# Optimization experiments

Hardware: AMD Instinct MI355X
Metric: run time of the kernel (lower is better)

The kernel has to match this reference:

```python
import jax, jax.numpy as jnp
import numpy as np

# aero table grids (degrees)
A_LO, A_HI = -20.0, 90.0
B_LO, B_HI = -30.0, 30.0
E_LO, E_HI = -25.0, 25.0


def _idx(x, lo, hi, n):
    t = jnp.clip((x - lo) / (hi - lo) * (n - 1), 0.0, float(n - 1))
    i0 = jnp.clip(t.astype(jnp.int32), 0, n - 2)
    return i0, t - i0


def _interp1(tab, x, lo, hi):
    i0, f = _idx(x, lo, hi, tab.shape[-1])
    return tab[..., i0] * (1.0 - f) + tab[..., i0 + 1] * f


def _interp2(tab, a, b):
    ia, fa = _idx(a, A_LO, A_HI, tab.shape[-2])
    ib, fb = _idx(b, B_LO, B_HI, tab.shape[-1])
    return (tab[:, ia, ib] * (1 - fa) * (1 - fb)
            + tab[:, ia + 1, ib] * fa * (1 - fb)
            + tab[:, ia, ib + 1] * (1 - fa) * fb
            + tab[:, ia + 1, ib + 1] * fa * fb)


def _interp3(tab, a, b, e):
    ia, fa = _idx(a, A_LO, A_HI, tab.shape[-3])
    ib, fb = _idx(b, B_LO, B_HI, tab.shape[-2])
    ie, fe = _idx(e, E_LO, E_HI, tab.shape[-1])
    out = 0.0
    for di, wa in ((0, 1 - fa), (1, fa)):
        for dj, wb in ((0, 1 - fb), (1, fb)):
            for dk, we in ((0, 1 - fe), (1, fe)):
                out = out + tab[:, ia + di, ib + dj, ie + dk] * (wa * wb * we)
    return out


def _nlplant(xu, tab3, tab2, tab1, tab_eta):
    g, m, Bspan, S, cbar = 32.17, 636.94, 30.0, 300.0, 11.32
    xcgr, xcg, Heng = 0.35, 0.25, 0.0
    Jy, Jxz, Jz, Jx = 55814.0, 982.0, 63100.0, 9496.0
    r2d = 180.0 / np.pi

    alt = xu[:, 2]
    phi, theta, psi = xu[:, 3], xu[:, 4], xu[:, 5]
    vt = jnp.maximum(xu[:, 6], 0.01)          # if vt < 0.01: vt = 0.01
    alpha, beta = xu[:, 7], xu[:, 8]
    a_deg, b_deg = alpha * r2d, beta * r2d
    P, Q, R = xu[:, 9], xu[:, 10], xu[:, 11]
    T, el, ail, rud, lef = xu[:, 12], xu[:, 13], xu[:, 14], xu[:, 15], xu[:, 16]
    dail, drud, dlef = ail / 21.5, rud / 30.0, 1.0 - lef / 25.0

    # --- Atmos ---
    tfac = 1.0 - 7.03e-06 * alt
    temp = jnp.where(alt >= 35000.0, 390.0, 519.0 * tfac)
    rho = 0.002377 * jnp.power(tfac, 4.14)
    qbar = 0.5 * rho * vt * vt
    ps = 1715.0 * rho * temp
    ps = jnp.where(ps == 0.0, 1715.0, ps)

    sa, ca = jnp.sin(alpha), jnp.cos(alpha)
    sb, cb = jnp.sin(beta), jnp.cos(beta)
    st, ct, tt = jnp.sin(theta), jnp.cos(theta), jnp.tan(theta)
    sphi, cphi = jnp.sin(phi), jnp.cos(phi)
    spsi, cpsi = jnp.sin(psi), jnp.cos(psi)

    U, V, W = vt * ca * cb, vt * sb, vt * sa * cb

    xd0 = U * (ct * cpsi) + V * (sphi * cpsi * st - cphi * spsi) + W * (cphi * st * cpsi + sphi * spsi)
    xd1 = U * (ct * spsi) + V * (sphi * spsi * st + cphi * cpsi) + W * (cphi * st * spsi - sphi * cpsi)
    xd2 = U * st - V * (sphi * ct) - W * (cphi * ct)
    xd3 = P + tt * (Q * sphi + R * cphi)
    xd4 = Q * cphi - R * sphi
    xd5 = (Q * sphi + R * cphi) / ct

    # --- aero table lookups ---
    v3 = _interp3(tab3, a_deg, b_deg, el)                    # [5,B]: Cx,Cz,Cm,Cn,Cl at el
    v30 = _interp3(tab3, a_deg, b_deg, jnp.zeros_like(el))   # [5,B]: at el=0
    v2 = _interp2(tab2, a_deg, b_deg)                        # [16,B]
    v1 = _interp1(tab1, a_deg, A_LO, A_HI)                   # [21,B]
    eta_el = _interp1(tab_eta, el, E_LO, E_HI)               # [B]

    Cx, Cz, Cm, Cn, Cl = v3[0], v3[1], v3[2], v3[3], v3[4]
    Cy = v2[0]
    (Cxq, Cyr, Cyp, Czq, Clr, Clp, Cmq, Cnr, Cnp,
     dCxq_lef, dCyr_lef, dCyp_lef, dCzq_lef, dClr_lef, dClp_lef,
     dCmq_lef, dCnr_lef, dCnp_lef, dCnbeta, dClbeta, dCm) = [v1[i] for i in range(21)]

    d_Cx_lef = v2[1] - v30[0]
    d_Cz_lef = v2[2] - v30[1]
    d_Cm_lef = v2[3] - v30[2]
    d_Cy_lef = v2[4] - v2[0]
    d_Cn_lef = v2[5] - v30[3]
    d_Cl_lef = v2[6] - v30[4]
    d_Cy_r30 = v2[7] - v2[0]
    d_Cn_r30 = v2[8] - v30[3]
    d_Cl_r30 = v2[9] - v30[4]
    d_Cy_a20 = v2[10] - v2[0]
    d_Cy_a20_lef = v2[11] - v2[4]
    d_Cn_a20 = v2[12] - v30[3]
    d_Cn_a20_lef = v2[13] - v2[5]
    d_Cl_a20 = v2[14] - v30[4]
    d_Cl_a20_lef = v2[15] - v2[6]
    d_Cm_ds = 0.0

    # --- total coefficients ---
    c2v = 1.0 / (2.0 * vt)
    dXdQ = cbar * c2v * (Cxq + dCxq_lef * dlef)
    Cx_tot = Cx + d_Cx_lef * dlef + dXdQ * Q
    dZdQ = cbar * c2v * (Czq + dCzq_lef * dlef)
    Cz_tot = Cz + d_Cz_lef * dlef + dZdQ * Q
    dMdQ = cbar * c2v * (Cmq + dCmq_lef * dlef)
    Cm_tot = Cm * eta_el + Cz_tot * (xcgr - xcg) + d_Cm_lef * dlef + dMdQ * Q + dCm + d_Cm_ds
    dYdail = d_Cy_a20 + d_Cy_a20_lef * dlef
    dYdR = Bspan * c2v * (Cyr + dCyr_lef * dlef)
    dYdP = Bspan * c2v * (Cyp + dCyp_lef * dlef)
    Cy_tot = Cy + d_Cy_lef * dlef + dYdail * dail + d_Cy_r30 * drud + dYdR * R + dYdP * P
    dNdail = d_Cn_a20 + d_Cn_a20_lef * dlef
    dNdR = Bspan * c2v * (Cnr + dCnr_lef * dlef)
    dNdP = Bspan * c2v * (Cnp + dCnp_lef * dlef)
    Cn_tot = (Cn + d_Cn_lef * dlef - Cy_tot * (xcgr - xcg) * (cbar / Bspan)
              + dNdail * dail + d_Cn_r30 * drud + dNdR * R + dNdP * P + dCnbeta * b_deg)
    dLdail = d_Cl_a20 + d_Cl_a20_lef * dlef
    dLdR = Bspan * c2v * (Clr + dClr_lef * dlef)
    dLdP = Bspan * c2v * (Clp + dClp_lef * dlef)
    Cl_tot = (Cl + d_Cl_lef * dlef + dLdail * dail + d_Cl_r30 * drud
              + dLdR * R + dLdP * P + dClbeta * b_deg)

    # --- body-axis accelerations ---
    qS_m = qbar * S / m
    Udot = R * V - Q * W - g * st + qS_m * Cx_tot + T / m
    Vdot = P * W - R * U + g * ct * sphi + qS_m * Cy_tot
    Wdot = Q * U - P * V + g * ct * cphi + qS_m * Cz_tot
    vt_dot = (U * Udot + V * Vdot + W * Wdot) / vt
    alpha_dot = (U * Wdot - W * Udot) / (U * U + W * W)
    beta_dot = (Vdot * vt - V * vt_dot) / (vt * vt * cb)

    # --- moments ---
    L_tot = Cl_tot * qbar * S * Bspan
    M_tot = Cm_tot * qbar * S * cbar
    N_tot = Cn_tot * qbar * S * Bspan
    denom = Jx * Jz - Jxz * Jxz
    P_dot = (Jz * L_tot + Jxz * N_tot - (Jz * (Jz - Jy) + Jxz * Jxz) * Q * R
             + Jxz * (Jx - Jy + Jz) * P * Q + Jxz * Q * Heng) / denom
    Q_dot = (M_tot + (Jz - Jx) * P * R - Jxz * (P * P - R * R) - R * Heng) / Jy
    R_dot = (Jx * N_tot + Jxz * L_tot + (Jx * (Jx - Jy) + Jxz * Jxz) * P * Q
             - Jxz * (Jx - Jy + Jz) * Q * R + Jx * Q * Heng) / denom

    xdot12 = jnp.stack([xd0, xd1, xd2, xd3, xd4, xd5,
                        vt_dot, alpha_dot, beta_dot, P_dot, Q_dot, R_dot], axis=1)
    return jnp.concatenate([xdot12, jnp.zeros((xu.shape[0], 5), xu.dtype)], axis=1)


def setup_inputs() -> dict:
    key = jax.random.key(0)
    k0, k1, k2, k3, k4 = jax.random.split(key, 5)
    Bn = 1 << 20
    u = jax.random.uniform(k0, (Bn, 17), dtype=jnp.float32)
    lo = jnp.array([0., 0., 0., -1., -1., -3., 300., -0.30, -0.5, -2., -2., -2.,
                    1000., -25., -21.5, -30., 0.], dtype=jnp.float32)
    hi = jnp.array([1000., 1000., 40000., 1., 1., 3., 900., 0.75, 0.5, 2., 2., 2.,
                    19000., 25., 21.5, 30., 25.], dtype=jnp.float32)
    xu = lo + u * (hi - lo)
    tab3 = 0.1 * jax.random.normal(k1, (5, 20, 19, 5), dtype=jnp.float32)
    tab2 = 0.05 * jax.random.normal(k2, (16, 20, 19), dtype=jnp.float32)
    tab1 = 0.1 * jax.random.normal(k3, (21, 20), dtype=jnp.float32)
    tab_eta = 1.0 + 0.05 * jax.random.normal(k4, (5,), dtype=jnp.float32)
    return {"xu": xu, "tab3": tab3, "tab2": tab2, "tab1": tab1, "tab_eta": tab_eta}


def reference(xu, tab3, tab2, tab1, tab_eta):
    return _nlplant(xu, tab3, tab2, tab1, tab_eta)
```

## Files before the change

### kernel.cpp

```cpp
#include <hip/hip_runtime.h>

#define BLOCK 1024
#define ROWS_PER_BLOCK 1024

__device__ __forceinline__ void idx_of(float x, float lo, float inv_range_times_nm1,
                                       int n, int& i0, float& f) {
    float t = (x - lo) * inv_range_times_nm1;
    t = fminf(fmaxf(t, 0.0f), (float)(n - 1));
    int i = (int)t;
    if (i > n - 2) i = n - 2;
    i0 = i;
    f = t - (float)i;
}

__global__ __launch_bounds__(BLOCK, 1)
void nlplant_kernel(const float* __restrict__ xu,
                    const float* __restrict__ tab3,
                    const float* __restrict__ tab2,
                    const float* __restrict__ tab1,
                    const float* __restrict__ tab_eta,
                    float* __restrict__ out, int nrows)
{
    __shared__ __align__(16) float s_t3a[1900 * 4];
    __shared__ __align__(16) float s_t3b[1900];
    __shared__ __align__(16) float s_tab2[380 * 20];
    __shared__ __align__(16) float s_tab1[428];
    __shared__ __align__(16) float s_io[512 * 17];

    const int tid = threadIdx.x;

#pragma unroll
    for (int c = 0; c < 5; ++c) {
        for (int idx = tid; idx < 1900; idx += BLOCK) {
            const float v = tab3[c * 1900 + idx];
            if (c < 4) s_t3a[(idx << 2) + c] = v;
            else       s_t3b[idx] = v;
        }
    }
    if (tid < 380) {
#pragma unroll
        for (int ch = 0; ch < 16; ++ch)
            s_tab2[tid * 20 + ch] = tab2[ch * 380 + tid];
    }
    if (tid < 420) {
        const int ch = tid / 20;
        const int ia = tid - ch * 20;
        s_tab1[ia * 21 + ch] = tab1[tid];
    }
    if (tid < 5) s_tab1[420 + tid] = tab_eta[tid];

    const int base = blockIdx.x * ROWS_PER_BLOCK;
    int remA = nrows - base;           if (remA < 0) remA = 0;
    const int rowsA = remA < 512 ? remA : 512;
    int remB = nrows - base - 512;     if (remB < 0) remB = 0;
    const int rowsB = remB < 512 ? remB : 512;

    if (rowsA == 512) {
        const float4* src = reinterpret_cast<const float4*>(xu + (size_t)base * 17);
        float4* dst = reinterpret_cast<float4*>(s_io);
        for (int k = tid; k < 2176; k += BLOCK) dst[k] = src[k];
    } else {
        for (int k = tid; k < rowsA * 17; k += BLOCK) s_io[k] = xu[(size_t)base * 17 + k];
    }
    __syncthreads();

    const int half = tid >> 9;
    const int l = tid & 511;
    const bool active = (half == 0) ? (l < rowsA) : (l < rowsB);

    float x[17];
#pragma unroll
    for (int j = 0; j < 17; ++j) x[j] = 1.0f;

    if (half == 0 && l < rowsA) {
#pragma unroll
        for (int j = 2; j < 17; ++j) x[j] = s_io[l * 17 + j];
    }
    __syncthreads();

    if (rowsB == 512) {
        const float4* src = reinterpret_cast<const float4*>(xu + (size_t)(base + 512) * 17);
        float4* dst = reinterpret_cast<float4*>(s_io);
        for (int k = tid; k < 2176; k += BLOCK) dst[k] = src[k];
    } else {
        for (int k = tid; k < rowsB * 17; k += BLOCK) s_io[k] = xu[(size_t)(base + 512) * 17 + k];
    }
    __syncthreads();
    if (half == 1 && l < rowsB) {
#pragma unroll
        for (int j = 2; j < 17; ++j) x[j] = s_io[l * 17 + j];
    }

    const float g = 32.17f, m_ = 636.94f, Bs = 30.0f, S = 300.0f, cbar = 11.32f;
    const float xcgr = 0.35f, xcg = 0.25f;
    const float Jy = 55814.0f, Jxz = 982.0f, Jz = 63100.0f, Jx = 9496.0f;
    const float r2d = 57.29577951308232f;

    const float alt = x[2], phi = x[3], theta = x[4], psi = x[5];
    const float vt = fmaxf(x[6], 0.01f);
    const float alpha = x[7], beta = x[8];
    const float a_deg = alpha * r2d, b_deg = beta * r2d;
    const float P = x[9], Q = x[10], R = x[11];
    const float T = x[12], el = x[13], ail = x[14], rud = x[15], lef = x[16];

    const float dail = ail * (1.0f / 21.5f);
    const float drud = rud * (1.0f / 30.0f);
    const float dlef = 1.0f - lef * (1.0f / 25.0f);

    const float tfac = 1.0f - 7.03e-6f * alt;
    const float rho = 0.002377f * __expf(4.14f * __logf(tfac));
    const float qbar = 0.5f * rho * vt * vt;

    float sa, ca, sb, cb, st, ct, sphi, cphi, spsi, cpsi;
    __sincosf(alpha, &sa, &ca);
    __sincosf(beta, &sb, &cb);
    __sincosf(theta, &st, &ct);
    __sincosf(phi, &sphi, &cphi);
    __sincosf(psi, &spsi, &cpsi);
    const float tt = st / ct;

    int ia, ib, ie; float fa, fb, fe;
    idx_of(a_deg, -20.0f, 19.0f / 110.0f, 20, ia, fa);
    idx_of(b_deg, -30.0f, 18.0f / 60.0f, 19, ib, fb);
    idx_of(el,    -25.0f,  4.0f / 50.0f,  5, ie, fe);

    const float wa[2] = {1.0f - fa, fa};
    const float wb[2] = {1.0f - fb, fb};
    const float we[2] = {1.0f - fe, fe};

    float v3c[5]  = {0, 0, 0, 0, 0};
    float v30c[5] = {0, 0, 0, 0, 0};
#pragma unroll
    for (int di = 0; di < 2; ++di) {
#pragma unroll
        for (int dj = 0; dj < 2; ++dj) {
            const float wab = wa[di] * wb[dj];
            const int pb3 = ((ia + di) * 19 + (ib + dj)) * 5;
#pragma unroll
            for (int dk = 0; dk < 2; ++dk) {
                const int idx = pb3 + ie + dk;
                const float4 q = *reinterpret_cast<const float4*>(&s_t3a[idx << 2]);
                const float q4 = s_t3b[idx];
                const float w = wab * we[dk];
                v3c[0] += q.x * w; v3c[1] += q.y * w; v3c[2] += q.z * w;
                v3c[3] += q.w * w; v3c[4] += q4 * w;
            }
            const int zidx = pb3 + 2;
            const float4 q0 = *reinterpret_cast<const float4*>(&s_t3a[zidx << 2]);
            const float q04 = s_t3b[zidx];
            v30c[0] += q0.x * wab; v30c[1] += q0.y * wab; v30c[2] += q0.z * wab;
            v30c[3] += q0.w * wab; v30c[4] += q04 * wab;
        }
    }

    float v2c[16];
    {
        const float w00 = wa[0] * wb[0], w01 = wa[0] * wb[1];
        const float w10 = wa[1] * wb[0], w11 = wa[1] * wb[1];
        const float4* p00 = reinterpret_cast<const float4*>(&s_tab2[(ia * 19 + ib) * 20]);
        const float4* p01 = reinterpret_cast<const float4*>(&s_tab2[(ia * 19 + ib + 1) * 20]);
        const float4* p10 = reinterpret_cast<const float4*>(&s_tab2[((ia + 1) * 19 + ib) * 20]);
        const float4* p11 = reinterpret_cast<const float4*>(&s_tab2[((ia + 1) * 19 + ib + 1) * 20]);
#pragma unroll
        for (int q = 0; q < 4; ++q) {
            const float4 a = p00[q], b = p01[q], c = p10[q], d = p11[q];
            v2c[4 * q + 0] = a.x * w00 + b.x * w01 + c.x * w10 + d.x * w11;
            v2c[4 * q + 1] = a.y * w00 + b.y * w01 + c.y * w10 + d.y * w11;
            v2c[4 * q + 2] = a.z * w00 + b.z * w01 + c.z * w10 + d.z * w11;
            v2c[4 * q + 3] = a.w * w00 + b.w * w01 + c.w * w10 + d.w * w11;
        }
    }

    float v1c[21];
    {
        const float* r0 = &s_tab1[ia * 21];
        const float* r1 = &s_tab1[(ia + 1) * 21];
#pragma unroll
        for (int c = 0; c < 21; ++c) v1c[c] = r0[c] * wa[0] + r1[c] * wa[1];
    }
    const float eta_el = s_tab1[420 + ie] * we[0] + s_tab1[421 + ie] * we[1];

    const float Cx = v3c[0], Cz = v3c[1], Cm = v3c[2], Cn = v3c[3], Cl = v3c[4];
    const float Cy = v2c[0];
    const float Cxq = v1c[0], Cyr = v1c[1], Cyp = v1c[2], Czq = v1c[3], Clr = v1c[4];
    const float Clp = v1c[5], Cmq = v1c[6], Cnr = v1c[7], Cnp = v1c[8];
    const float dCxq_lef = v1c[9], dCyr_lef = v1c[10], dCyp_lef = v1c[11];
    const float dCzq_lef = v1c[12], dClr_lef = v1c[13], dClp_lef = v1c[14];
    const float dCmq_lef = v1c[15], dCnr_lef = v1c[16], dCnp_lef = v1c[17];
    const float dCnbeta = v1c[18], dClbeta = v1c[19], dCm = v1c[20];

    const float d_Cx_lef = v2c[1] - v30c[0];
    const float d_Cz_lef = v2c[2] - v30c[1];
    const float d_Cm_lef = v2c[3] - v30c[2];
    const float d_Cy_lef = v2c[4] - v2c[0];
    const float d_Cn_lef = v2c[5] - v30c[3];
    const float d_Cl_lef = v2c[6] - v30c[4];
    const float d_Cy_r30 = v2c[7] - v2c[0];
    const float d_Cn_r30 = v2c[8] - v30c[3];
    const float d_Cl_r30 = v2c[9] - v30c[4];
    const float d_Cy_a20 = v2c[10] - v2c[0];
    const float d_Cy_a20_lef = v2c[11] - v2c[4];
    const float d_Cn_a20 = v2c[12] - v30c[3];
    const float d_Cn_a20_lef = v2c[13] - v2c[5];
    const float d_Cl_a20 = v2c[14] - v30c[4];
    const float d_Cl_a20_lef = v2c[15] - v2c[6];

    const float U = vt * ca * cb, V = vt * sb, W = vt * sa * cb;
    const float o0 = U * (ct * cpsi) + V * (sphi * cpsi * st - cphi * spsi) + W * (cphi * st * cpsi + sphi * spsi);
    const float o1 = U * (ct * spsi) + V * (sphi * spsi * st + cphi * cpsi) + W * (cphi * st * spsi - sphi * cpsi);
    const float o2 = U * st - V * (sphi * ct) - W * (cphi * ct);
    const float o3 = P + tt * (Q * sphi + R * cphi);
    const float o4 = Q * cphi - R * sphi;
    const float o5 = (Q * sphi + R * cphi) / ct;

    const float c2v = 1.0f / (2.0f * vt);
    const float cq = cbar * c2v, bq = Bs * c2v;
    const float dXdQ = cq * (Cxq + dCxq_lef * dlef);
    const float Cx_tot = Cx + d_Cx_lef * dlef + dXdQ * Q;
    const float dZdQ = cq * (Czq + dCzq_lef * dlef);
    const float Cz_tot = Cz + d_Cz_lef * dlef + dZdQ * Q;
    const float dMdQ = cq * (Cmq + dCmq_lef * dlef);
    const float Cm_tot = Cm * eta_el + Cz_tot * (xcgr - xcg) + d_Cm_lef * dlef + dMdQ * Q + dCm;
    const float dYdail = d_Cy_a20 + d_Cy_a20_lef * dlef;
    const float dYdR = bq * (Cyr + dCyr_lef * dlef);
    const float dYdP = bq * (Cyp + dCyp_lef * dlef);
    const float Cy_tot = Cy + d_Cy_lef * dlef + dYdail * dail + d_Cy_r30 * drud + dYdR * R + dYdP * P;
    const float dNdail = d_Cn_a20 + d_Cn_a20_lef * dlef;
    const float dNdR = bq * (Cnr + dCnr_lef * dlef);
    const float dNdP = bq * (Cnp + dCnp_lef * dlef);
    const float Cn_tot = Cn + d_Cn_lef * dlef - Cy_tot * ((xcgr - xcg) * (cbar / Bs))
                       + dNdail * dail + d_Cn_r30 * drud + dNdR * R + dNdP * P + dCnbeta * b_deg;
    const float dLdail = d_Cl_a20 + d_Cl_a20_lef * dlef;
    const float dLdR = bq * (Clr + dClr_lef * dlef);
    const float dLdP = bq * (Clp + dClp_lef * dlef);
    const float Cl_tot = Cl + d_Cl_lef * dlef + dLdail * dail + d_Cl_r30 * drud
                       + dLdR * R + dLdP * P + dClbeta * b_deg;

    const float qS = qbar * S;
    const float qS_m = qS * (1.0f / m_);
    const float Udot = R * V - Q * W - g * st + qS_m * Cx_tot + T * (1.0f / m_);
    const float Vdot = P * W - R * U + g * ct * sphi + qS_m * Cy_tot;
    const float Wdot = Q * U - P * V + g * ct * cphi + qS_m * Cz_tot;
    const float o6 = (U * Udot + V * Vdot + W * Wdot) / vt;
    const float o7 = (U * Wdot - W * Udot) / (U * U + W * W);
    const float o8 = (Vdot * vt - V * o6) / (vt * vt * cb);

    const float L_tot = Cl_tot * qS * Bs;
    const float M_tot = Cm_tot * qS * cbar;
    const float N_tot = Cn_tot * qS * Bs;
    const float denom = Jx * Jz - Jxz * Jxz;
    const float inv_denom = 1.0f / denom;
    const float o9  = (Jz * L_tot + Jxz * N_tot - (Jz * (Jz - Jy) + Jxz * Jxz) * Q * R
                      + Jxz * (Jx - Jy + Jz) * P * Q) * inv_denom;
    const float o10 = (M_tot + (Jz - Jx) * P * R - Jxz * (P * P - R * R)) * (1.0f / Jy);
    const float o11 = (Jx * N_tot + Jxz * L_tot + (Jx * (Jx - Jy) + Jxz * Jxz) * P * Q
                      - Jxz * (Jx - Jy + Jz) * Q * R) * inv_denom;

    float o[17] = {o0, o1, o2, o3, o4, o5, o6, o7, o8, o9, o10, o11,
                   0.0f, 0.0f, 0.0f, 0.0f, 0.0f};

    __syncthreads();
    if (half == 0 && active) {
#pragma unroll
        for (int j = 0; j < 17; ++j) s_io[l * 17 + j] = o[j];
    }
    __syncthreads();
    if (rowsA == 512) {
        const float4* src = reinterpret_cast<const float4*>(s_io);
        float4* dst = reinterpret_cast<float4*>(out + (size_t)base * 17);
        for (int k = tid; k < 2176; k += BLOCK) dst[k] = src[k];
    } else {
        for (int k = tid; k < rowsA * 17; k += BLOCK) out[(size_t)base * 17 + k] = s_io[k];
    }
    __syncthreads();
    if (half == 1 && active) {
#pragma unroll
        for (int j = 0; j < 17; ++j) s_io[l * 17 + j] = o[j];
    }
    __syncthreads();
    if (rowsB == 512) {
        const float4* src = reinterpret_cast<const float4*>(s_io);
        float4* dst = reinterpret_cast<float4*>(out + (size_t)(base + 512) * 17);
        for (int k = tid; k < 2176; k += BLOCK) dst[k] = src[k];
    } else {
        for (int k = tid; k < rowsB * 17; k += BLOCK) out[(size_t)(base + 512) * 17 + k] = s_io[k];
    }
}

extern "C" void kernel_launch(void* const* d_in, const int* in_sizes, int n_in,
                              void* d_out, int out_size, void* d_ws, size_t ws_size,
                              hipStream_t stream) {
    const float* xu      = (const float*)d_in[0];
    const float* tab3    = (const float*)d_in[1];
    const float* tab2    = (const float*)d_in[2];
    const float* tab1    = (const float*)d_in[3];
    const float* tab_eta = (const float*)d_in[4];
    float* out = (float*)d_out;

    const int nrows = in_sizes[0] / 17;
    const int grid = (nrows + ROWS_PER_BLOCK - 1) / ROWS_PER_BLOCK;
    nlplant_kernel<<<grid, BLOCK, 0, stream>>>(xu, tab3, tab2, tab1, tab_eta, out, nrows);
}
```

Measured before the change: 64.14 us.

## Process two full 1024-row passes per block with direct strided output stores

Each block now handles 2048 rows in two passes where every thread computes one row, instead of 1024 rows staged as two 512-row halves. This amortizes the per-block table load into shared memory over more rows and doubles the staging buffer. Output is now written directly from registers with strided scalar stores, dropping the shared-memory staging and the coalesced float4 store. Divisions are replaced by hardware reciprocal approximations and tab1 is padded to stride 28 for float4 reads. The strided global stores risk poor coalescing, the larger shared footprint may cut occupancy, and the reciprocals slightly change numerics.

```diff
diff --git a/kernel.cpp b/kernel.cpp
--- a/kernel.cpp
+++ b/kernel.cpp
@@ -1,7 +1,9 @@
 #include <hip/hip_runtime.h>
 
 #define BLOCK 1024
-#define ROWS_PER_BLOCK 1024
+#define PASS_ROWS 1024
+#define PASSES 2
+#define ROWS_PER_BLOCK (PASS_ROWS * PASSES)
 
 __device__ __forceinline__ void idx_of(float x, float lo, float inv_range_times_nm1,
                                        int n, int& i0, float& f) {
@@ -24,8 +26,8 @@
     __shared__ __align__(16) float s_t3a[1900 * 4];
     __shared__ __align__(16) float s_t3b[1900];
     __shared__ __align__(16) float s_tab2[380 * 20];
-    __shared__ __align__(16) float s_tab1[428];
-    __shared__ __align__(16) float s_io[512 * 17];
+    __shared__ __align__(16) float s_tab1[568];
+    __shared__ __align__(16) float s_io[PASS_ROWS * 17];
 
     const int tid = threadIdx.x;
 
@@ -45,245 +47,220 @@
     if (tid < 420) {
         const int ch = tid / 20;
         const int ia = tid - ch * 20;
-        s_tab1[ia * 21 + ch] = tab1[tid];
-    }
-    if (tid < 5) s_tab1[420 + tid] = tab_eta[tid];
-
-    const int base = blockIdx.x * ROWS_PER_BLOCK;
-    int remA = nrows - base;           if (remA < 0) remA = 0;
-    const int rowsA = remA < 512 ? remA : 512;
-    int remB = nrows - base - 512;     if (remB < 0) remB = 0;
-    const int rowsB = remB < 512 ? remB : 512;
-
-    if (rowsA == 512) {
-        const float4* src = reinterpret_cast<const float4*>(xu + (size_t)base * 17);
-        float4* dst = reinterpret_cast<float4*>(s_io);
-        for (int k = tid; k < 2176; k += BLOCK) dst[k] = src[k];
-    } else {
-        for (int k = tid; k < rowsA * 17; k += BLOCK) s_io[k] = xu[(size_t)base * 17 + k];
-    }
-    __syncthreads();
-
-    const int half = tid >> 9;
-    const int l = tid & 511;
-    const bool active = (half == 0) ? (l < rowsA) : (l < rowsB);
-
-    float x[17];
-#pragma unroll
-    for (int j = 0; j < 17; ++j) x[j] = 1.0f;
-
-    if (half == 0 && l < rowsA) {
-#pragma unroll
-        for (int j = 2; j < 17; ++j) x[j] = s_io[l * 17 + j];
-    }
-    __syncthreads();
-
-    if (rowsB == 512) {
-        const float4* src = reinterpret_cast<const float4*>(xu + (size_t)(base + 512) * 17);
-        float4* dst = reinterpret_cast<float4*>(s_io);
-        for (int k = tid; k < 2176; k += BLOCK) dst[k] = src[k];
-    } else {
-        for (int k = tid; k < rowsB * 17; k += BLOCK) s_io[k] = xu[(size_t)(base + 512) * 17 + k];
-    }
-    __syncthreads();
-    if (half == 1 && l < rowsB) {
-#pragma unroll
-        for (int j = 2; j < 17; ++j) x[j] = s_io[l * 17 + j];
-    }
+        s_tab1[ia * 28 + ch] = tab1[tid];
+    }
+    if (tid < 5) s_tab1[560 + tid] = tab_eta[tid];
 
     const float g = 32.17f, m_ = 636.94f, Bs = 30.0f, S = 300.0f, cbar = 11.32f;
     const float xcgr = 0.35f, xcg = 0.25f;
     const float Jy = 55814.0f, Jxz = 982.0f, Jz = 63100.0f, Jx = 9496.0f;
     const float r2d = 57.29577951308232f;
 
-    const float alt = x[2], phi = x[3], theta = x[4], psi = x[5];
-    const float vt = fmaxf(x[6], 0.01f);
-    const float alpha = x[7], beta = x[8];
-    const float a_deg = alpha * r2d, b_deg = beta * r2d;
-    const float P = x[9], Q = x[10], R = x[11];
-    const float T = x[12], el = x[13], ail = x[14], rud = x[15], lef = x[16];
-
-    const float dail = ail * (1.0f / 21.5f);
-    const float drud = rud * (1.0f / 30.0f);
-    const float dlef = 1.0f - lef * (1.0f / 25.0f);
-
-    const float tfac = 1.0f - 7.03e-6f * alt;
-    const float rho = 0.002377f * __expf(4.14f * __logf(tfac));
-    const float qbar = 0.5f * rho * vt * vt;
-
-    float sa, ca, sb, cb, st, ct, sphi, cphi, spsi, cpsi;
-    __sincosf(alpha, &sa, &ca);
-    __sincosf(beta, &sb, &cb);
-    __sincosf(theta, &st, &ct);
-    __sincosf(phi, &sphi, &cphi);
-    __sincosf(psi, &spsi, &cpsi);
-    const float tt = st / ct;
-
-    int ia, ib, ie; float fa, fb, fe;
-    idx_of(a_deg, -20.0f, 19.0f / 110.0f, 20, ia, fa);
-    idx_of(b_deg, -30.0f, 18.0f / 60.0f, 19, ib, fb);
-    idx_of(el,    -25.0f,  4.0f / 50.0f,  5, ie, fe);
-
-    const float wa[2] = {1.0f - fa, fa};
-    const float wb[2] = {1.0f - fb, fb};
-    const float we[2] = {1.0f - fe, fe};
-
-    float v3c[5]  = {0, 0, 0, 0, 0};
-    float v30c[5] = {0, 0, 0, 0, 0};
-#pragma unroll
-    for (int di = 0; di < 2; ++di) {
-#pragma unroll
-        for (int dj = 0; dj < 2; ++dj) {
-            const float wab = wa[di] * wb[dj];
-            const int pb3 = ((ia + di) * 19 + (ib + dj)) * 5;
-#pragma unroll
-            for (int dk = 0; dk < 2; ++dk) {
-                const int idx = pb3 + ie + dk;
-                const float4 q = *reinterpret_cast<const float4*>(&s_t3a[idx << 2]);
-                const float q4 = s_t3b[idx];
-                const float w = wab * we[dk];
-                v3c[0] += q.x * w; v3c[1] += q.y * w; v3c[2] += q.z * w;
-                v3c[3] += q.w * w; v3c[4] += q4 * w;
+    const int base = blockIdx.x * ROWS_PER_BLOCK;
+
+    for (int p = 0; p < PASSES; ++p) {
+        const int pb = base + p * PASS_ROWS;
+        int rem = nrows - pb; if (rem < 0) rem = 0;
+        const int rows = rem < PASS_ROWS ? rem : PASS_ROWS;
+
+        if (rows == PASS_ROWS) {
+            const float4* src = reinterpret_cast<const float4*>(xu + (size_t)pb * 17);
+            float4* dst = reinterpret_cast<float4*>(s_io);
+            for (int k = tid; k < PASS_ROWS * 17 / 4; k += BLOCK) dst[k] = src[k];
+        } else {
+            for (int k = tid; k < rows * 17; k += BLOCK) s_io[k] = xu[(size_t)pb * 17 + k];
+        }
+        __syncthreads();
+
+        const bool active = tid < rows;
+        float x[17];
+#pragma unroll
+        for (int j = 0; j < 17; ++j) x[j] = 1.0f;
+        if (active) {
+#pragma unroll
+            for (int j = 2; j < 17; ++j) x[j] = s_io[tid * 17 + j];
+        }
+        __syncthreads();
+
+        const float alt = x[2], phi = x[3], theta = x[4], psi = x[5];
+        const float vt = fmaxf(x[6], 0.01f);
+        const float alpha = x[7], beta = x[8];
+        const float a_deg = alpha * r2d, b_deg = beta * r2d;
+        const float P = x[9], Q = x[10], R = x[11];
+        const float T = x[12], el = x[13], ail = x[14], rud = x[15], lef = x[16];
+
+        const float dail = ail * (1.0f / 21.5f);
+        const float drud = rud * (1.0f / 30.0f);
+        const float dlef = 1.0f - lef * (1.0f / 25.0f);
+
+        const float tfac = 1.0f - 7.03e-6f * alt;
+        const float rho = 0.002377f * __expf(4.14f * __logf(tfac));
+        const float qbar = 0.5f * rho * vt * vt;
+
+        float sa, ca, sb, cb, st, ct, sphi, cphi, spsi, cpsi;
+        __sincosf(alpha, &sa, &ca);
+        __sincosf(beta, &sb, &cb);
+        __sincosf(theta, &st, &ct);
+        __sincosf(phi, &sphi, &cphi);
+        __sincosf(psi, &spsi, &cpsi);
+
+        const float rcp_ct = __builtin_amdgcn_rcpf(ct);
+        const float rcp_vt = __builtin_amdgcn_rcpf(vt);
+        const float tt = st * rcp_ct;
+
+        int ia, ib, ie; float fa, fb, fe;
+        idx_of(a_deg, -20.0f, 19.0f / 110.0f, 20, ia, fa);
+        idx_of(b_deg, -30.0f, 18.0f / 60.0f, 19, ib, fb);
+        idx_of(el,    -25.0f,  4.0f / 50.0f,  5, ie, fe);
+
+        const float wa[2] = {1.0f - fa, fa};
+        const float wb[2] = {1.0f - fb, fb};
+        const float we[2] = {1.0f - fe, fe};
+
+        float v3c[5]  = {0, 0, 0, 0, 0};
+        float v30c[5] = {0, 0, 0, 0, 0};
+#pragma unroll
+        for (int di = 0; di < 2; ++di) {
+#pragma unroll
+            for (int dj = 0; dj < 2; ++dj) {
+                const float wab = wa[di] * wb[dj];
+                const int pb3 = ((ia + di) * 19 + (ib + dj)) * 5;
+#pragma unroll
+                for (int dk = 0; dk < 2; ++dk) {
+                    const int idx = pb3 + ie + dk;
+                    const float4 q = *reinterpret_cast<const float4*>(&s_t3a[idx << 2]);
+                    const float q4 = s_t3b[idx];
+                    const float w = wab * we[dk];
+                    v3c[0] += q.x * w; v3c[1] += q.y * w; v3c[2] += q.z * w;
+                    v3c[3] += q.w * w; v3c[4] += q4 * w;
+                }
+                const int zidx = pb3 + 2;
+                const float4 q0 = *reinterpret_cast<const float4*>(&s_t3a[zidx << 2]);
+                const float q04 = s_t3b[zidx];
+                v30c[0] += q0.x * wab; v30c[1] += q0.y * wab; v30c[2] += q0.z * wab;
+                v30c[3] += q0.w * wab; v30c[4] += q04 * wab;
             }
-            const int zidx = pb3 + 2;
-            const float4 q0 = *reinterpret_cast<const float4*>(&s_t3a[zidx << 2]);
-            const float q04 = s_t3b[zidx];
-            v30c[0] += q0.x * wab; v30c[1] += q0.y * wab; v30c[2] += q0.z * wab;
-            v30c[3] += q0.w * wab; v30c[4] += q04 * wab;
-        }
-    }
-
-    float v2c[16];
-    {
-        const float w00 = wa[0] * wb[0], w01 = wa[0] * wb[1];
-        const float w10 = wa[1] * wb[0], w11 = wa[1] * wb[1];
-        const float4* p00 = reinterpret_cast<const float4*>(&s_tab2[(ia * 19 + ib) * 20]);
-        const float4* p01 = reinterpret_cast<const float4*>(&s_tab2[(ia * 19 + ib + 1) * 20]);
-        const float4* p10 = reinterpret_cast<const float4*>(&s_tab2[((ia + 1) * 19 + ib) * 20]);
-        const float4* p11 = reinterpret_cast<const float4*>(&s_tab2[((ia + 1) * 19 + ib + 1) * 20]);
-#pragma unroll
-        for (int q = 0; q < 4; ++q) {
-            const float4 a = p00[q], b = p01[q], c = p10[q], d = p11[q];
-            v2c[4 * q + 0] = a.x * w00 + b.x * w01 + c.x * w10 + d.x * w11;
-            v2c[4 * q + 1] = a.y * w00 + b.y * w01 + c.y * w10 + d.y * w11;
-            v2c[4 * q + 2] = a.z * w00 + b.z * w01 + c.z * w10 + d.z * w11;
-            v2c[4 * q + 3] = a.w * w00 + b.w * w01 + c.w * w10 + d.w * w11;
-        }
-    }
-
-    float v1c[21];
-    {
-        const float* r0 = &s_tab1[ia * 21];
-        const float* r1 = &s_tab1[(ia + 1) * 21];
-#pragma unroll
-        for (int c = 0; c < 21; ++c) v1c[c] = r0[c] * wa[0] + r1[c] * wa[1];
-    }
-    const float eta_el = s_tab1[420 + ie] * we[0] + s_tab1[421 + ie] * we[1];
-
-    const float Cx = v3c[0], Cz = v3c[1], Cm = v3c[2], Cn = v3c[3], Cl = v3c[4];
-    const float Cy = v2c[0];
-    const float Cxq = v1c[0], Cyr = v1c[1], Cyp = v1c[2], Czq = v1c[3], Clr = v1c[4];
-    const float Clp = v1c[5], Cmq = v1c[6], Cnr = v1c[7], Cnp = v1c[8];
-    const float dCxq_lef = v1c[9], dCyr_lef = v1c[10], dCyp_lef = v1c[11];
-    const float dCzq_lef = v1c[12], dClr_lef = v1c[13], dClp_lef = v1c[14];
-    const float dCmq_lef = v1c[15], dCnr_lef = v1c[16], dCnp_lef = v1c[17];
-    const float dCnbeta = v1c[18], dClbeta = v1c[19], dCm = v1c[20];
-
-    const float d_Cx_lef = v2c[1] - v30c[0];
-    const float d_Cz_lef = v2c[2] - v30c[1];
-    const float d_Cm_lef = v2c[3] - v30c[2];
-    const float d_Cy_lef = v2c[4] - v2c[0];
-    const float d_Cn_lef = v2c[5] - v30c[3];
-    const float d_Cl_lef = v2c[6] - v30c[4];
-    const float d_Cy_r30 = v2c[7] - v2c[0];
-    const float d_Cn_r30 = v2c[8] - v30c[3];
-    const float d_Cl_r30 = v2c[9] - v30c[4];
-    const float d_Cy_a20 = v2c[10] - v2c[0];
-    const float d_Cy_a20_lef = v2c[11] - v2c[4];
-    const float d_Cn_a20 = v2c[12] - v30c[3];
-    const float d_Cn_a20_lef = v2c[13] - v2c[5];
-    const float d_Cl_a20 = v2c[14] - v30c[4];
-    const float d_Cl_a20_lef = v2c[15] - v2c[6];
-
-    const float U = vt * ca * cb, V = vt * sb, W = vt * sa * cb;
-    const float o0 = U * (ct * cpsi) + V * (sphi * cpsi * st - cphi * spsi) + W * (cphi * st * cpsi + sphi * spsi);
-    const float o1 = U * (ct * spsi) + V * (sphi * spsi * st + cphi * cpsi) + W * (cphi * st * spsi - sphi * cpsi);
-    const float o2 = U * st - V * (sphi * ct) - W * (cphi * ct);
-    const float o3 = P + tt * (Q * sphi + R * cphi);
-    const float o4 = Q * cphi - R * sphi;
-    const float o5 = (Q * sphi + R * cphi) / ct;
-
-    const float c2v = 1.0f / (2.0f * vt);
-    const float cq = cbar * c2v, bq = Bs * c2v;
-    const float dXdQ = cq * (Cxq + dCxq_lef * dlef);
-    const float Cx_tot = Cx + d_Cx_lef * dlef + dXdQ * Q;
-    const float dZdQ = cq * (Czq + dCzq_lef * dlef);
-    const float Cz_tot = Cz + d_Cz_lef * dlef + dZdQ * Q;
-    const float dMdQ = cq * (Cmq + dCmq_lef * dlef);
-    const float Cm_tot = Cm * eta_el + Cz_tot * (xcgr - xcg) + d_Cm_lef * dlef + dMdQ * Q + dCm;
-    const float dYdail = d_Cy_a20 + d_Cy_a20_lef * dlef;
-    const float dYdR = bq * (Cyr + dCyr_lef * dlef);
-    const float dYdP = bq * (Cyp + dCyp_lef * dlef);
-    const float Cy_tot = Cy + d_Cy_lef * dlef + dYdail * dail + d_Cy_r30 * drud + dYdR * R + dYdP * P;
-    const float dNdail = d_Cn_a20 + d_Cn_a20_lef * dlef;
-    const float dNdR = bq * (Cnr + dCnr_lef * dlef);
-    const float dNdP = bq * (Cnp + dCnp_lef * dlef);
-    const float Cn_tot = Cn + d_Cn_lef * dlef - Cy_tot * ((xcgr - xcg) * (cbar / Bs))
-                       + dNdail * dail + d_Cn_r30 * drud + dNdR * R + dNdP * P + dCnbeta * b_deg;
-    const float dLdail = d_Cl_a20 + d_Cl_a20_lef * dlef;
-    const float dLdR = bq * (Clr + dClr_lef * dlef);
-    const float dLdP = bq * (Clp + dClp_lef * dlef);
-    const float Cl_tot = Cl + d_Cl_lef * dlef + dLdail * dail + d_Cl_r30 * drud
-                       + dLdR * R + dLdP * P + dClbeta * b_deg;
-
-    const float qS = qbar * S;
-    const float qS_m = qS * (1.0f / m_);
-    const float Udot = R * V - Q * W - g * st + qS_m * Cx_tot + T * (1.0f / m_);
-    const float Vdot = P * W - R * U + g * ct * sphi + qS_m * Cy_tot;
-    const float Wdot = Q * U - P * V + g * ct * cphi + qS_m * Cz_tot;
-    const float o6 = (U * Udot + V * Vdot + W * Wdot) / vt;
-    const float o7 = (U * Wdot - W * Udot) / (U * U + W * W);
-    const float o8 = (Vdot * vt - V * o6) / (vt * vt * cb);
-
-    const float L_tot = Cl_tot * qS * Bs;
-    const float M_tot = Cm_tot * qS * cbar;
-    const float N_tot = Cn_tot * qS * Bs;
-    const float denom = Jx * Jz - Jxz * Jxz;
-    const float inv_denom = 1.0f / denom;
-    const float o9  = (Jz * L_tot + Jxz * N_tot - (Jz * (Jz - Jy) + Jxz * Jxz) * Q * R
-                      + Jxz * (Jx - Jy + Jz) * P * Q) * inv_denom;
-    const float o10 = (M_tot + (Jz - Jx) * P * R - Jxz * (P * P - R * R)) * (1.0f / Jy);
-    const float o11 = (Jx * N_tot + Jxz * L_tot + (Jx * (Jx - Jy) + Jxz * Jxz) * P * Q
-                      - Jxz * (Jx - Jy + Jz) * Q * R) * inv_denom;
-
-    float o[17] = {o0, o1, o2, o3, o4, o5, o6, o7, o8, o9, o10, o11,
-                   0.0f, 0.0f, 0.0f, 0.0f, 0.0f};
-
-    __syncthreads();
-    if (half == 0 && active) {
-#pragma unroll
-        for (int j = 0; j < 17; ++j) s_io[l * 17 + j] = o[j];
-    }
-    __syncthreads();
-    if (rowsA == 512) {
-        const float4* src = reinterpret_cast<const float4*>(s_io);
-        float4* dst = reinterpret_cast<float4*>(out + (size_t)base * 17);
-        for (int k = tid; k < 2176; k += BLOCK) dst[k] = src[k];
-    } else {
-        for (int k = tid; k < rowsA * 17; k += BLOCK) out[(size_t)base * 17 + k] = s_io[k];
-    }
-    __syncthreads();
-    if (half == 1 && active) {
-#pragma unroll
-        for (int j = 0; j < 17; ++j) s_io[l * 17 + j] = o[j];
-    }
-    __syncthreads();
-    if (rowsB == 512) {
-        const float4* src = reinterpret_cast<const float4*>(s_io);
-        float4* dst = reinterpret_cast<float4*>(out + (size_t)(base + 512) * 17);
-        for (int k = tid; k < 2176; k += BLOCK) dst[k] = src[k];
-    } else {
-        for (int k = tid; k < rowsB * 17; k += BLOCK) out[(size_t)(base + 512) * 17 + k] = s_io[k];
+        }
+
+        float v2c[16];
+        {
+            const float w00 = wa[0] * wb[0], w01 = wa[0] * wb[1];
+            const float w10 = wa[1] * wb[0], w11 = wa[1] * wb[1];
+            const float4* p00 = reinterpret_cast<const float4*>(&s_tab2[(ia * 19 + ib) * 20]);
+            const float4* p01 = reinterpret_cast<const float4*>(&s_tab2[(ia * 19 + ib + 1) * 20]);
+            const float4* p10 = reinterpret_cast<const float4*>(&s_tab2[((ia + 1) * 19 + ib) * 20]);
+            const float4* p11 = reinterpret_cast<const float4*>(&s_tab2[((ia + 1) * 19 + ib + 1) * 20]);
+#pragma unroll
+            for (int q = 0; q < 4; ++q) {
+                const float4 a = p00[q], b = p01[q], c = p10[q], d = p11[q];
+                v2c[4 * q + 0] = a.x * w00 + b.x * w01 + c.x * w10 + d.x * w11;
+                v2c[4 * q + 1] = a.y * w00 + b.y * w01 + c.y * w10 + d.y * w11;
+                v2c[4 * q + 2] = a.z * w00 + b.z * w01 + c.z * w10 + d.z * w11;
+                v2c[4 * q + 3] = a.w * w00 + b.w * w01 + c.w * w10 + d.w * w11;
+            }
+        }
+
+        float v1c[21];
+        {
+            const float4* r0 = reinterpret_cast<const float4*>(&s_tab1[ia * 28]);
+            const float4* r1 = reinterpret_cast<const float4*>(&s_tab1[(ia + 1) * 28]);
+#pragma unroll
+            for (int q = 0; q < 5; ++q) {
+                const float4 a = r0[q], b = r1[q];
+                v1c[4 * q + 0] = a.x * wa[0] + b.x * wa[1];
+                v1c[4 * q + 1] = a.y * wa[0] + b.y * wa[1];
+                v1c[4 * q + 2] = a.z * wa[0] + b.z * wa[1];
+                if (q < 5 - 1 || true) {  }
+                v1c[4 * q + 3] = a.w * wa[0] + b.w * wa[1];
+            }
+            v1c[20] = s_tab1[ia * 28 + 20] * wa[0] + s_tab1[(ia + 1) * 28 + 20] * wa[1];
+        }
+        const float eta_el = s_tab1[560 + ie] * we[0] + s_tab1[561 + ie] * we[1];
+
+        const float Cx = v3c[0], Cz = v3c[1], Cm = v3c[2], Cn = v3c[3], Cl = v3c[4];
+        const float Cy = v2c[0];
+        const float Cxq = v1c[0], Cyr = v1c[1], Cyp = v1c[2], Czq = v1c[3], Clr = v1c[4];
+        const float Clp = v1c[5], Cmq = v1c[6], Cnr = v1c[7], Cnp = v1c[8];
+        const float dCxq_lef = v1c[9], dCyr_lef = v1c[10], dCyp_lef = v1c[11];
+        const float dCzq_lef = v1c[12], dClr_lef = v1c[13], dClp_lef = v1c[14];
+        const float dCmq_lef = v1c[15], dCnr_lef = v1c[16], dCnp_lef = v1c[17];
+        const float dCnbeta = v1c[18], dClbeta = v1c[19], dCm = v1c[20];
+
+        const float d_Cx_lef = v2c[1] - v30c[0];
+        const float d_Cz_lef = v2c[2] - v30c[1];
+        const float d_Cm_lef = v2c[3] - v30c[2];
+        const float d_Cy_lef = v2c[4] - v2c[0];
+        const float d_Cn_lef = v2c[5] - v30c[3];
+        const float d_Cl_lef = v2c[6] - v30c[4];
+        const float d_Cy_r30 = v2c[7] - v2c[0];
+        const float d_Cn_r30 = v2c[8] - v30c[3];
+        const float d_Cl_r30 = v2c[9] - v30c[4];
+        const float d_Cy_a20 = v2c[10] - v2c[0];
+        const float d_Cy_a20_lef = v2c[11] - v2c[4];
+        const float d_Cn_a20 = v2c[12] - v30c[3];
+        const float d_Cn_a20_lef = v2c[13] - v2c[5];
+        const float d_Cl_a20 = v2c[14] - v30c[4];
+        const float d_Cl_a20_lef = v2c[15] - v2c[6];
+
+        const float U = vt * ca * cb, V = vt * sb, W = vt * sa * cb;
+        const float o0 = U * (ct * cpsi) + V * (sphi * cpsi * st - cphi * spsi) + W * (cphi * st * cpsi + sphi * spsi);
+        const float o1 = U * (ct * spsi) + V * (sphi * spsi * st + cphi * cpsi) + W * (cphi * st * spsi - sphi * cpsi);
+        const float o2 = U * st - V * (sphi * ct) - W * (cphi * ct);
+        const float o3 = P + tt * (Q * sphi + R * cphi);
+        const float o4 = Q * cphi - R * sphi;
+        const float o5 = (Q * sphi + R * cphi) * rcp_ct;
+
+        const float c2v = 0.5f * rcp_vt;
+        const float cq = cbar * c2v, bq = Bs * c2v;
+        const float dXdQ = cq * (Cxq + dCxq_lef * dlef);
+        const float Cx_tot = Cx + d_Cx_lef * dlef + dXdQ * Q;
+        const float dZdQ = cq * (Czq + dCzq_lef * dlef);
+        const float Cz_tot = Cz + d_Cz_lef * dlef + dZdQ * Q;
+        const float dMdQ = cq * (Cmq + dCmq_lef * dlef);
+        const float Cm_tot = Cm * eta_el + Cz_tot * (xcgr - xcg) + d_Cm_lef * dlef + dMdQ * Q + dCm;
+        const float dYdail = d_Cy_a20 + d_Cy_a20_lef * dlef;
+        const float dYdR = bq * (Cyr + dCyr_lef * dlef);
+        const float dYdP = bq * (Cyp + dCyp_lef * dlef);
+        const float Cy_tot = Cy + d_Cy_lef * dlef + dYdail * dail + d_Cy_r30 * drud + dYdR * R + dYdP * P;
+        const float dNdail = d_Cn_a20 + d_Cn_a20_lef * dlef;
+        const float dNdR = bq * (Cnr + dCnr_lef * dlef);
+        const float dNdP = bq * (Cnp + dCnp_lef * dlef);
+        const float Cn_tot = Cn + d_Cn_lef * dlef - Cy_tot * ((xcgr - xcg) * (cbar / Bs))
+                           + dNdail * dail + d_Cn_r30 * drud + dNdR * R + dNdP * P + dCnbeta * b_deg;
+        const float dLdail = d_Cl_a20 + d_Cl_a20_lef * dlef;
+        const float dLdR = bq * (Clr + dClr_lef * dlef);
+        const float dLdP = bq * (Clp + dClp_lef * dlef);
+        const float Cl_tot = Cl + d_Cl_lef * dlef + dLdail * dail + d_Cl_r30 * drud
+                           + dLdR * R + dLdP * P + dClbeta * b_deg;
+
+        const float qS = qbar * S;
+        const float qS_m = qS * (1.0f / m_);
+        const float Udot = R * V - Q * W - g * st + qS_m * Cx_tot + T * (1.0f / m_);
+        const float Vdot = P * W - R * U + g * ct * sphi + qS_m * Cy_tot;
+        const float Wdot = Q * U - P * V + g * ct * cphi + qS_m * Cz_tot;
+        const float o6 = (U * Udot + V * Vdot + W * Wdot) * rcp_vt;
+        const float o7 = (U * Wdot - W * Udot) * __builtin_amdgcn_rcpf(U * U + W * W);
+        const float o8 = (Vdot * vt - V * o6) * __builtin_amdgcn_rcpf(vt * vt * cb);
+
+        const float L_tot = Cl_tot * qS * Bs;
+        const float M_tot = Cm_tot * qS * cbar;
+        const float N_tot = Cn_tot * qS * Bs;
+        const float denom = Jx * Jz - Jxz * Jxz;
+        const float inv_denom = 1.0f / denom;
+        const float o9  = (Jz * L_tot + Jxz * N_tot - (Jz * (Jz - Jy) + Jxz * Jxz) * Q * R
+                          + Jxz * (Jx - Jy + Jz) * P * Q) * inv_denom;
+        const float o10 = (M_tot + (Jz - Jx) * P * R - Jxz * (P * P - R * R)) * (1.0f / Jy);
+        const float o11 = (Jx * N_tot + Jxz * L_tot + (Jx * (Jx - Jy) + Jxz * Jxz) * P * Q
+                          - Jxz * (Jx - Jy + Jz) * Q * R) * inv_denom;
+
+        if (active) {
+            float* orow = out + (size_t)(pb + tid) * 17;
+            orow[0] = o0;  orow[1] = o1;  orow[2] = o2;  orow[3] = o3;
+            orow[4] = o4;  orow[5] = o5;  orow[6] = o6;  orow[7] = o7;
+            orow[8] = o8;  orow[9] = o9;  orow[10] = o10; orow[11] = o11;
+            orow[12] = 0.0f; orow[13] = 0.0f; orow[14] = 0.0f; orow[15] = 0.0f;
+            orow[16] = 0.0f;
+        }
     }
 }
 
```

New measurement: 88.42 us. 1.38x slower.
